# Performance work log

Hardware: AMD Instinct MI355X
Metric: run time of the kernel (lower is better)

## Reference

```python
import jax, jax.numpy as jnp
import numpy as np

N = 100000      # nodes
D = 128         # num_hidden_channels == num_output_feats
H = 4           # attention heads
HD = D // H     # head dim = 32
KNN = 20        # in-edges per node
E = N * KNN
BN_EPS = 1e-5


def setup_inputs() -> dict:
    key = jax.random.key(0)
    ks = jax.random.split(key, 20)
    s = 1.0 / np.sqrt(D)
    f = jax.random.normal(ks[0], (N, D), jnp.float32)
    src = jax.random.randint(ks[1], (E,), 0, N, dtype=jnp.int32)
    dst = jnp.repeat(jnp.arange(N, dtype=jnp.int32), KNN)  # knn in-edges per node
    return {
        "f": f,
        "src": src,
        "dst": dst,
        "bn1_gamma": jax.random.normal(ks[2], (D,), jnp.float32) * 0.1 + 1.0,
        "bn1_beta": jax.random.normal(ks[3], (D,), jnp.float32) * 0.1,
        "bn1_mean": jax.random.normal(ks[4], (D,), jnp.float32) * 0.1,
        "bn1_var": jax.random.uniform(ks[5], (D,), jnp.float32, 0.5, 1.5),
        "Wq": jax.random.normal(ks[6], (D, D), jnp.float32) * s,
        "Wk": jax.random.normal(ks[7], (D, D), jnp.float32) * s,
        "Wv": jax.random.normal(ks[8], (D, D), jnp.float32) * s,
        "Wo": jax.random.normal(ks[9], (D, D), jnp.float32) * s,
        "bo": jax.random.normal(ks[10], (D,), jnp.float32) * 0.01,
        "bn2_gamma": jax.random.normal(ks[11], (D,), jnp.float32) * 0.1 + 1.0,
        "bn2_beta": jax.random.normal(ks[12], (D,), jnp.float32) * 0.1,
        "bn2_mean": jax.random.normal(ks[13], (D,), jnp.float32) * 0.1,
        "bn2_var": jax.random.uniform(ks[14], (D,), jnp.float32, 0.5, 1.5),
        "W1": jax.random.normal(ks[15], (D, 2 * D), jnp.float32) * s,
        "W2": jax.random.normal(ks[16], (2 * D, D), jnp.float32) * (1.0 / np.sqrt(2 * D)),
    }


def _bn(x, gamma, beta, mean, var):
    # eval-mode BatchNorm1d with running statistics
    return (x - mean) * (gamma / jnp.sqrt(var + BN_EPS)) + beta


def reference(f, src, dst, bn1_gamma, bn1_beta, bn1_mean, bn1_var,
              Wq, Wk, Wv, Wo, bo,
              bn2_gamma, bn2_beta, bn2_mean, bn2_var, W1, W2):
    n = f.shape[0]
    h = _bn(f, bn1_gamma, bn1_beta, bn1_mean, bn1_var)
    q = (h @ Wq).reshape(n, H, HD)
    k = (h @ Wk).reshape(n, H, HD)
    v = (h @ Wv).reshape(n, H, HD)
    # edge-wise score: K[src] . Q[dst]  -> [E, H]
    score = jnp.einsum('ehd,ehd->eh', k[src], q[dst]) / np.sqrt(HD)
    score = jnp.exp(jnp.clip(score, -5.0, 5.0))
    # scatter-sum weighted V and normalizer to destination nodes
    wV = jax.ops.segment_sum(v[src] * score[:, :, None], dst, num_segments=n)  # [N,H,HD]
    z = jax.ops.segment_sum(score, dst, num_segments=n)                        # [N,H]
    attn = (wV / (z[:, :, None] + 1e-6)).reshape(n, D)
    node = attn @ Wo + bo
    node = f + node  # residual 1 (dropout is identity in eval)
    h2 = _bn(node, bn2_gamma, bn2_beta, bn2_mean, bn2_var)
    mlp = jax.nn.silu(h2 @ W1) @ W2
    return node + mlp  # residual 2
```

## Files before the change

kernel.cpp:

```cpp
#include <hip/hip_runtime.h>
#include <hip/hip_bf16.h>

#define NN 100000
#define DD 128
#define KNN 20

typedef unsigned short u16;
typedef __attribute__((ext_vector_type(8))) __bf16 bf16x8;
typedef __attribute__((ext_vector_type(4))) float f32x4;
typedef __attribute__((ext_vector_type(4))) unsigned short u16x4;
typedef __attribute__((ext_vector_type(8))) unsigned short u16x8;

__device__ __forceinline__ float b2f(u16 b) {
  unsigned int u = ((unsigned int)b) << 16;
  float f;
  __builtin_memcpy(&f, &u, 4);
  return f;
}
__device__ __forceinline__ u16 f2b(float f) {
  unsigned int u;
  __builtin_memcpy(&u, &f, 4);
  u += 0x7fffu + ((u >> 16) & 1u);
  return (u16)(u >> 16);
}

__global__ __launch_bounds__(256) void bn1_kernel(
    const float* __restrict__ f, const float* __restrict__ g, const float* __restrict__ be,
    const float* __restrict__ mu, const float* __restrict__ va, u16* __restrict__ h)
{
  int idx = (blockIdx.x * 256 + threadIdx.x) * 8;
  if (idx >= NN * DD) return;
  int c = idx & (DD - 1);
  u16x8 out;
#pragma unroll
  for (int j = 0; j < 8; j++) {
    float scale = g[c + j] * rsqrtf(va[c + j] + 1e-5f);
    out[j] = f2b((f[idx + j] - mu[c + j]) * scale + be[c + j]);
  }
  *(u16x8*)(h + idx) = out;
}

__device__ __forceinline__ void stage_frag(const float* __restrict__ W, int wstride,
                                           int colbase, u16* __restrict__ dst, int f) {
  int lane = f & 63;
  int t2 = f >> 6;
  int ksl = t2 & 3;
  int ct = (t2 >> 2) & 7;
  int kc = t2 >> 5;
  int ks = kc * 4 + ksl;
  int quad = lane >> 4, l16 = lane & 15;
  const float* src = W + (size_t)(ks * 32 + quad * 8) * wstride + colbase + ct * 16 + l16;
  u16x8 o;
#pragma unroll
  for (int j = 0; j < 8; j++) o[j] = f2b(src[(size_t)j * wstride]);
  *(u16x8*)(dst + (size_t)f * 8) = o;
}

__global__ __launch_bounds__(256) void stage_weights_kernel(
    const float* __restrict__ Wq, const float* __restrict__ Wk, const float* __restrict__ Wv,
    const float* __restrict__ Wo, const float* __restrict__ W1, const float* __restrict__ W2,
    u16* __restrict__ WTf)
{
  int t = blockIdx.x * 256 + threadIdx.x;
  if (t < 2048)       stage_frag(Wq, 128, 0,   WTf + 0,     t);
  else if (t < 4096)  stage_frag(Wk, 128, 0,   WTf + 16384, t - 2048);
  else if (t < 6144)  stage_frag(Wv, 128, 0,   WTf + 32768, t - 4096);
  else if (t < 8192)  stage_frag(Wo, 128, 0,   WTf + 49152, t - 6144);
  else if (t < 10240) stage_frag(W1, 256, 0,   WTf + 65536, t - 8192);
  else if (t < 12288) stage_frag(W1, 256, 128, WTf + 81920, t - 10240);
  else if (t < 16384) stage_frag(W2, 128, 0,   WTf + 98304, t - 12288);
}

template <int K, int NB, int MODE>
__global__ __launch_bounds__(256) void gemm3_kernel(
    const u16* __restrict__ A, const u16* __restrict__ Bf,
    u16* __restrict__ o0, u16* __restrict__ o1,
    float* __restrict__ of, float* __restrict__ nodef,
    const float* __restrict__ fres, const float* __restrict__ bo,
    const float* __restrict__ g2, const float* __restrict__ b2,
    const float* __restrict__ m2, const float* __restrict__ v2,
    const float* __restrict__ nodein, int nrows)
{
  constexpr int KS = K / 32;
  constexpr int NC = K / 128;
  __shared__ u16 Bs[16384];
  const int tid = threadIdx.x;
  const int wave = tid >> 6;
  const int lane = tid & 63;
  const int quad = lane >> 4;
  const int l16 = lane & 15;
  const int rowbase = blockIdx.x * 128 + wave * 32;

  bf16x8 a[2][KS];
#pragma unroll
  for (int rt = 0; rt < 2; rt++) {
    int arow = rowbase + rt * 16 + l16;
    if (arow >= nrows) arow = nrows - 1;
    const u16* Ap = A + (size_t)arow * K + quad * 8;
#pragma unroll
    for (int ks = 0; ks < KS; ks++) a[rt][ks] = *(const bf16x8*)(Ap + ks * 32);
  }

#pragma unroll
  for (int m = 0; m < NB; m++) {
    const u16* Bm = Bf + (size_t)m * (128 * K);
    f32x4 acc[2][8];
#pragma unroll
    for (int rt = 0; rt < 2; rt++)
#pragma unroll
      for (int ct = 0; ct < 8; ct++) acc[rt][ct] = (f32x4){0.f, 0.f, 0.f, 0.f};

#pragma unroll
    for (int kc = 0; kc < NC; kc++) {
      __syncthreads();
      const u16* srcp = Bm + kc * 16384 + tid * 8;
#pragma unroll
      for (int i = 0; i < 8; i++)
        *(u16x8*)(Bs + i * 2048 + tid * 8) = *(const u16x8*)(srcp + i * 2048);
      __syncthreads();
#pragma unroll
      for (int ct = 0; ct < 8; ct++) {
#pragma unroll
        for (int ksl = 0; ksl < 4; ksl++) {
          bf16x8 b = *(const bf16x8*)(Bs + ((ct * 4 + ksl) * 64 + lane) * 8);
          acc[0][ct] = __builtin_amdgcn_mfma_f32_16x16x32_bf16(a[0][kc * 4 + ksl], b, acc[0][ct], 0, 0, 0);
          acc[1][ct] = __builtin_amdgcn_mfma_f32_16x16x32_bf16(a[1][kc * 4 + ksl], b, acc[1][ct], 0, 0, 0);
        }
      }
    }

#pragma unroll
    for (int rt = 0; rt < 2; rt++) {
#pragma unroll
      for (int ct = 0; ct < 8; ct++) {
        int coll = ct * 16 + l16;
#pragma unroll
        for (int r = 0; r < 4; r++) {
          int row = rowbase + rt * 16 + quad * 4 + r;
          if (row >= nrows) continue;
          float val = acc[rt][ct][r];
          if (MODE == 0) {
            if (m == 0) o0[(size_t)row * DD + coll] = f2b(val);
            else if (m == 1) o1[(size_t)row * 256 + coll * 2] = f2b(val);
            else o1[(size_t)row * 256 + coll * 2 + 1] = f2b(val);
          } else if (MODE == 1) {
            float nv = val + bo[coll] + fres[(size_t)row * DD + coll];
            nodef[(size_t)row * DD + coll] = nv;
            float sc2 = g2[coll] * rsqrtf(v2[coll] + 1e-5f);
            o0[(size_t)row * DD + coll] = f2b((nv - m2[coll]) * sc2 + b2[coll]);
          } else if (MODE == 2) {
            int col = m * 128 + coll;
            float s = val / (1.f + __expf(-val));
            o0[(size_t)row * 256 + col] = f2b(s);
          } else {
            of[(size_t)row * DD + coll] = val + nodein[(size_t)row * DD + coll];
          }
        }
      }
    }
  }
}

__global__ __launch_bounds__(256) void attn_kernel(
    const u16* __restrict__ q, const u16* __restrict__ kv,
    const int* __restrict__ src, u16* __restrict__ attn)
{
  const int node = blockIdx.x * 8 + (threadIdx.x >> 5);
  const int sub = threadIdx.x & 31;
  const int c0 = sub * 4;
  const size_t qbase = (size_t)node * DD + c0;

  u16x4 qr = *(const u16x4*)(q + qbase);
  const float qv0 = b2f(qr[0]), qv1 = b2f(qr[1]), qv2 = b2f(qr[2]), qv3 = b2f(qr[3]);

  int sv[KNN];
  const int* sp = src + (size_t)node * KNN;
#pragma unroll
  for (int j = 0; j < KNN; j++) sv[j] = sp[j];

  float a0 = 0.f, a1 = 0.f, a2 = 0.f, a3 = 0.f, z = 0.f;
  const float inv_sqrt_hd = 0.17677669529663687f;
#pragma unroll
  for (int j = 0; j < KNN; j++) {
    u16x8 kvr = *(const u16x8*)(kv + (size_t)sv[j] * 256 + c0 * 2);
    float p = b2f(kvr[0]) * qv0 + b2f(kvr[2]) * qv1 + b2f(kvr[4]) * qv2 + b2f(kvr[6]) * qv3;
    p += __shfl_xor(p, 1);
    p += __shfl_xor(p, 2);
    p += __shfl_xor(p, 4);
    float sc = __expf(fminf(fmaxf(p * inv_sqrt_hd, -5.f), 5.f));
    z += sc;
    a0 += sc * b2f(kvr[1]);
    a1 += sc * b2f(kvr[3]);
    a2 += sc * b2f(kvr[5]);
    a3 += sc * b2f(kvr[7]);
  }
  float inv = 1.f / (z + 1e-6f);
  u16x4 o;
  o[0] = f2b(a0 * inv); o[1] = f2b(a1 * inv);
  o[2] = f2b(a2 * inv); o[3] = f2b(a3 * inv);
  *(u16x4*)(attn + qbase) = o;
}

extern "C" void kernel_launch(void* const* d_in, const int* in_sizes, int n_in,
                              void* d_out, int out_size, void* d_ws, size_t ws_size,
                              hipStream_t stream) {
  const float* f  = (const float*)d_in[0];
  const int* src  = (const int*)d_in[1];
  const float* g1 = (const float*)d_in[3];
  const float* b1 = (const float*)d_in[4];
  const float* m1 = (const float*)d_in[5];
  const float* v1 = (const float*)d_in[6];
  const float* Wq = (const float*)d_in[7];
  const float* Wk = (const float*)d_in[8];
  const float* Wv = (const float*)d_in[9];
  const float* Wo = (const float*)d_in[10];
  const float* bo = (const float*)d_in[11];
  const float* g2 = (const float*)d_in[12];
  const float* b2 = (const float*)d_in[13];
  const float* m2 = (const float*)d_in[14];
  const float* v2 = (const float*)d_in[15];
  const float* W1 = (const float*)d_in[16];
  const float* W2 = (const float*)d_in[17];
  float* out = (float*)d_out;

  char* ws = (char*)d_ws;
  const size_t SZ = (size_t)NN * DD * 2;
  u16*  h     = (u16*)(ws + 0);
  u16*  qb    = (u16*)(ws + SZ);
  u16*  kv    = (u16*)(ws + 2 * SZ);
  float* node = (float*)(ws + 4 * SZ);
  u16*  inter = (u16*)(ws + 2 * SZ);
  u16*  attn  = h;
  u16*  h2    = qb;
  u16*  WTf   = (u16*)(ws + 6 * SZ);

  const int g3grid = (NN + 127) / 128;

  bn1_kernel<<<(NN * DD / 8 + 255) / 256, 256, 0, stream>>>(f, g1, b1, m1, v1, h);
  stage_weights_kernel<<<64, 256, 0, stream>>>(Wq, Wk, Wv, Wo, W1, W2, WTf);

  gemm3_kernel<128, 3, 0><<<g3grid, 256, 0, stream>>>(
      h, WTf + 0, qb, kv, nullptr, nullptr,
      nullptr, nullptr, nullptr, nullptr, nullptr, nullptr, nullptr, NN);

  attn_kernel<<<NN / 8, 256, 0, stream>>>(qb, kv, src, attn);

  gemm3_kernel<128, 1, 1><<<g3grid, 256, 0, stream>>>(
      attn, WTf + 49152, h2, nullptr, nullptr, node,
      f, bo, g2, b2, m2, v2, nullptr, NN);

  gemm3_kernel<128, 2, 2><<<g3grid, 256, 0, stream>>>(
      h2, WTf + 65536, inter, nullptr, nullptr, nullptr,
      nullptr, nullptr, nullptr, nullptr, nullptr, nullptr, nullptr, NN);

  gemm3_kernel<256, 1, 3><<<g3grid, 256, 0, stream>>>(
      inter, WTf + 98304, nullptr, nullptr, out, nullptr,
      nullptr, nullptr, nullptr, nullptr, nullptr, nullptr, node, NN);
}
```

Measured before the change: 533.8 us.

## Fuse BN1 into QKV GEMM and fuse output, BN2 and MLP into one kernel

Folds BatchNorm1 into the QKV projection so the normalized activations are never written to memory, and fuses the Wo projection, residual, BN2, the SiLU MLP and the final residual into one kernel. The intermediate node and inter tensors stay in registers or per-wave shared-memory tiles instead of round-tripping through HBM. Weight fragments are now read straight from global/L2 instead of being staged into shared memory, and BN scale/bias are precomputed once. This removes several full-size intermediate reads and writes and some launches, in exchange for more register pressure in the fused MLP kernel and a partially unrolled attention loop.

Result: no change. 525.5 us (-1.6%).

```diff
diff --git a/kernel.cpp b/kernel.cpp
--- a/kernel.cpp
+++ b/kernel.cpp
@@ -22,22 +22,6 @@
   __builtin_memcpy(&u, &f, 4);
   u += 0x7fffu + ((u >> 16) & 1u);
   return (u16)(u >> 16);
-}
-
-__global__ __launch_bounds__(256) void bn1_kernel(
-    const float* __restrict__ f, const float* __restrict__ g, const float* __restrict__ be,
-    const float* __restrict__ mu, const float* __restrict__ va, u16* __restrict__ h)
-{
-  int idx = (blockIdx.x * 256 + threadIdx.x) * 8;
-  if (idx >= NN * DD) return;
-  int c = idx & (DD - 1);
-  u16x8 out;
-#pragma unroll
-  for (int j = 0; j < 8; j++) {
-    float scale = g[c + j] * rsqrtf(va[c + j] + 1e-5f);
-    out[j] = f2b((f[idx + j] - mu[c + j]) * scale + be[c + j]);
-  }
-  *(u16x8*)(h + idx) = out;
 }
 
 __device__ __forceinline__ void stage_frag(const float* __restrict__ W, int wstride,
@@ -59,7 +43,14 @@
 __global__ __launch_bounds__(256) void stage_weights_kernel(
     const float* __restrict__ Wq, const float* __restrict__ Wk, const float* __restrict__ Wv,
     const float* __restrict__ Wo, const float* __restrict__ W1, const float* __restrict__ W2,
-    u16* __restrict__ WTf)
+    const float* __restrict__ g1, const float* __restrict__ b1,
+    const float* __restrict__ m1, const float* __restrict__ v1,
+    const float* __restrict__ g2, const float* __restrict__ b2,
+    const float* __restrict__ m2, const float* __restrict__ v2,
+    const float* __restrict__ bo,
+    u16* __restrict__ WTf,
+    float* __restrict__ sc1, float* __restrict__ bb1,
+    float* __restrict__ sc2, float* __restrict__ bb2, float* __restrict__ bof)
 {
   int t = blockIdx.x * 256 + threadIdx.x;
   if (t < 2048)       stage_frag(Wq, 128, 0,   WTf + 0,     t);
@@ -69,101 +60,99 @@
   else if (t < 10240) stage_frag(W1, 256, 0,   WTf + 65536, t - 8192);
   else if (t < 12288) stage_frag(W1, 256, 128, WTf + 81920, t - 10240);
   else if (t < 16384) stage_frag(W2, 128, 0,   WTf + 98304, t - 12288);
-}
-
-template <int K, int NB, int MODE>
-__global__ __launch_bounds__(256) void gemm3_kernel(
-    const u16* __restrict__ A, const u16* __restrict__ Bf,
-    u16* __restrict__ o0, u16* __restrict__ o1,
-    float* __restrict__ of, float* __restrict__ nodef,
-    const float* __restrict__ fres, const float* __restrict__ bo,
-    const float* __restrict__ g2, const float* __restrict__ b2,
-    const float* __restrict__ m2, const float* __restrict__ v2,
-    const float* __restrict__ nodein, int nrows)
+  else if (t < 16512) {
+    int c = t - 16384;
+    float s1 = g1[c] * rsqrtf(v1[c] + 1e-5f);
+    sc1[c] = s1; bb1[c] = b1[c] - m1[c] * s1;
+    float s2 = g2[c] * rsqrtf(v2[c] + 1e-5f);
+    sc2[c] = s2; bb2[c] = b2[c] - m2[c] * s2;
+    bof[c] = bo[c];
+  }
+}
+
+__global__ __launch_bounds__(256) void qkv_kernel(
+    const float* __restrict__ f, const u16* __restrict__ WTf,
+    const float* __restrict__ sc1, const float* __restrict__ bb1,
+    u16* __restrict__ qb, u16* __restrict__ kvb)
 {
-  constexpr int KS = K / 32;
-  constexpr int NC = K / 128;
-  __shared__ u16 Bs[16384];
   const int tid = threadIdx.x;
-  const int wave = tid >> 6;
-  const int lane = tid & 63;
-  const int quad = lane >> 4;
-  const int l16 = lane & 15;
+  const int wave = tid >> 6, lane = tid & 63, quad = lane >> 4, l16 = lane & 15;
   const int rowbase = blockIdx.x * 128 + wave * 32;
 
-  bf16x8 a[2][KS];
-#pragma unroll
-  for (int rt = 0; rt < 2; rt++) {
-    int arow = rowbase + rt * 16 + l16;
-    if (arow >= nrows) arow = nrows - 1;
-    const u16* Ap = A + (size_t)arow * K + quad * 8;
-#pragma unroll
-    for (int ks = 0; ks < KS; ks++) a[rt][ks] = *(const bf16x8*)(Ap + ks * 32);
-  }
-
-#pragma unroll
-  for (int m = 0; m < NB; m++) {
-    const u16* Bm = Bf + (size_t)m * (128 * K);
+  bf16x8 af[2][4];
+#pragma unroll
+  for (int ks = 0; ks < 4; ks++) {
+    int ch = ks * 32 + quad * 8;
+    f32x4 s0 = *(const f32x4*)(sc1 + ch), s1 = *(const f32x4*)(sc1 + ch + 4);
+    f32x4 c0 = *(const f32x4*)(bb1 + ch), c1 = *(const f32x4*)(bb1 + ch + 4);
+#pragma unroll
+    for (int rt = 0; rt < 2; rt++) {
+      int arow = rowbase + rt * 16 + l16;
+      if (arow >= NN) arow = NN - 1;
+      const float* fp = f + (size_t)arow * DD + ch;
+      f32x4 x0 = *(const f32x4*)(fp), x1 = *(const f32x4*)(fp + 4);
+      u16x8 hv;
+#pragma unroll
+      for (int j = 0; j < 4; j++) {
+        hv[j]     = f2b(x0[j] * s0[j] + c0[j]);
+        hv[j + 4] = f2b(x1[j] * s1[j] + c1[j]);
+      }
+      af[rt][ks] = __builtin_bit_cast(bf16x8, hv);
+    }
+  }
+
+  u16x4 ks16[2][8];
+#pragma unroll
+  for (int m = 0; m < 3; m++) {
     f32x4 acc[2][8];
 #pragma unroll
     for (int rt = 0; rt < 2; rt++)
 #pragma unroll
       for (int ct = 0; ct < 8; ct++) acc[rt][ct] = (f32x4){0.f, 0.f, 0.f, 0.f};
-
-#pragma unroll
-    for (int kc = 0; kc < NC; kc++) {
-      __syncthreads();
-      const u16* srcp = Bm + kc * 16384 + tid * 8;
-#pragma unroll
-      for (int i = 0; i < 8; i++)
-        *(u16x8*)(Bs + i * 2048 + tid * 8) = *(const u16x8*)(srcp + i * 2048);
-      __syncthreads();
+#pragma unroll
+    for (int ct = 0; ct < 8; ct++)
+#pragma unroll
+      for (int ks = 0; ks < 4; ks++) {
+        bf16x8 wf = *(const bf16x8*)(WTf + (size_t)m * 16384 + ((ct * 4 + ks) * 64 + lane) * 8);
+        acc[0][ct] = __builtin_amdgcn_mfma_f32_16x16x32_bf16(wf, af[0][ks], acc[0][ct], 0, 0, 0);
+        acc[1][ct] = __builtin_amdgcn_mfma_f32_16x16x32_bf16(wf, af[1][ks], acc[1][ct], 0, 0, 0);
+      }
+#pragma unroll
+    for (int rt = 0; rt < 2; rt++)
 #pragma unroll
       for (int ct = 0; ct < 8; ct++) {
-#pragma unroll
-        for (int ksl = 0; ksl < 4; ksl++) {
-          bf16x8 b = *(const bf16x8*)(Bs + ((ct * 4 + ksl) * 64 + lane) * 8);
-          acc[0][ct] = __builtin_amdgcn_mfma_f32_16x16x32_bf16(a[0][kc * 4 + ksl], b, acc[0][ct], 0, 0, 0);
-          acc[1][ct] = __builtin_amdgcn_mfma_f32_16x16x32_bf16(a[1][kc * 4 + ksl], b, acc[1][ct], 0, 0, 0);
-        }
-      }
-    }
-
-#pragma unroll
-    for (int rt = 0; rt < 2; rt++) {
-#pragma unroll
-      for (int ct = 0; ct < 8; ct++) {
-        int coll = ct * 16 + l16;
-#pragma unroll
-        for (int r = 0; r < 4; r++) {
-          int row = rowbase + rt * 16 + quad * 4 + r;
-          if (row >= nrows) continue;
-          float val = acc[rt][ct][r];
-          if (MODE == 0) {
-            if (m == 0) o0[(size_t)row * DD + coll] = f2b(val);
-            else if (m == 1) o1[(size_t)row * 256 + coll * 2] = f2b(val);
-            else o1[(size_t)row * 256 + coll * 2 + 1] = f2b(val);
-          } else if (MODE == 1) {
-            float nv = val + bo[coll] + fres[(size_t)row * DD + coll];
-            nodef[(size_t)row * DD + coll] = nv;
-            float sc2 = g2[coll] * rsqrtf(v2[coll] + 1e-5f);
-            o0[(size_t)row * DD + coll] = f2b((nv - m2[coll]) * sc2 + b2[coll]);
-          } else if (MODE == 2) {
-            int col = m * 128 + coll;
-            float s = val / (1.f + __expf(-val));
-            o0[(size_t)row * 256 + col] = f2b(s);
-          } else {
-            of[(size_t)row * DD + coll] = val + nodein[(size_t)row * DD + coll];
+        int row = rowbase + rt * 16 + l16;
+        int ch0 = ct * 16 + quad * 4;
+        if (m == 0) {
+          if (row < NN) {
+            u16x4 o;
+#pragma unroll
+            for (int r = 0; r < 4; r++) o[r] = f2b(acc[rt][ct][r]);
+            *(u16x4*)(qb + (size_t)row * DD + ch0) = o;
+          }
+        } else if (m == 1) {
+          u16x4 o;
+#pragma unroll
+          for (int r = 0; r < 4; r++) o[r] = f2b(acc[rt][ct][r]);
+          ks16[rt][ct] = o;
+        } else {
+          if (row < NN) {
+            u16x8 o;
+#pragma unroll
+            for (int r = 0; r < 4; r++) {
+              o[2 * r] = ks16[rt][ct][r];
+              o[2 * r + 1] = f2b(acc[rt][ct][r]);
+            }
+            *(u16x8*)(kvb + (size_t)row * 256 + ch0 * 2) = o;
           }
         }
       }
-    }
   }
 }
 
 __global__ __launch_bounds__(256) void attn_kernel(
     const u16* __restrict__ q, const u16* __restrict__ kv,
-    const int* __restrict__ src, u16* __restrict__ attn)
+    const int* __restrict__ src, u16* __restrict__ attnb)
 {
   const int node = blockIdx.x * 8 + (threadIdx.x >> 5);
   const int sub = threadIdx.x & 31;
@@ -180,7 +169,7 @@
 
   float a0 = 0.f, a1 = 0.f, a2 = 0.f, a3 = 0.f, z = 0.f;
   const float inv_sqrt_hd = 0.17677669529663687f;
-#pragma unroll
+#pragma unroll 10
   for (int j = 0; j < KNN; j++) {
     u16x8 kvr = *(const u16x8*)(kv + (size_t)sv[j] * 256 + c0 * 2);
     float p = b2f(kvr[0]) * qv0 + b2f(kvr[2]) * qv1 + b2f(kvr[4]) * qv2 + b2f(kvr[6]) * qv3;
@@ -198,7 +187,134 @@
   u16x4 o;
   o[0] = f2b(a0 * inv); o[1] = f2b(a1 * inv);
   o[2] = f2b(a2 * inv); o[3] = f2b(a3 * inv);
-  *(u16x4*)(attn + qbase) = o;
+  *(u16x4*)(attnb + qbase) = o;
+}
+
+__global__ __launch_bounds__(256) void mlp_kernel(
+    const u16* __restrict__ attnb, const float* __restrict__ f, const u16* __restrict__ WTf,
+    const float* __restrict__ bof, const float* __restrict__ sc2, const float* __restrict__ bb2,
+    float* __restrict__ out)
+{
+  __shared__ u16 T[8704];
+  const int tid = threadIdx.x;
+  const int wave = tid >> 6, lane = tid & 63, quad = lane >> 4, l16 = lane & 15;
+  const int rowbase = blockIdx.x * 128 + wave * 32;
+  u16* tile = T + wave * 2176;
+
+  bf16x8 af[2][4];
+#pragma unroll
+  for (int rt = 0; rt < 2; rt++) {
+    int arow = rowbase + rt * 16 + l16;
+    if (arow >= NN) arow = NN - 1;
+    const u16* ap = attnb + (size_t)arow * DD + quad * 8;
+#pragma unroll
+    for (int ks = 0; ks < 4; ks++) af[rt][ks] = *(const bf16x8*)(ap + ks * 32);
+  }
+
+  f32x4 nv[2][8];
+#pragma unroll
+  for (int rt = 0; rt < 2; rt++)
+#pragma unroll
+    for (int ct = 0; ct < 8; ct++) nv[rt][ct] = (f32x4){0.f, 0.f, 0.f, 0.f};
+#pragma unroll
+  for (int ct = 0; ct < 8; ct++)
+#pragma unroll
+    for (int ks = 0; ks < 4; ks++) {
+      bf16x8 wf = *(const bf16x8*)(WTf + 49152 + ((ct * 4 + ks) * 64 + lane) * 8);
+      nv[0][ct] = __builtin_amdgcn_mfma_f32_16x16x32_bf16(wf, af[0][ks], nv[0][ct], 0, 0, 0);
+      nv[1][ct] = __builtin_amdgcn_mfma_f32_16x16x32_bf16(wf, af[1][ks], nv[1][ct], 0, 0, 0);
+    }
+
+  u16x4 h4s[8];
+#pragma unroll
+  for (int ct = 0; ct < 8; ct++) {
+    int ch0 = ct * 16 + quad * 4;
+    f32x4 bo4 = *(const f32x4*)(bof + ch0);
+    f32x4 s4  = *(const f32x4*)(sc2 + ch0);
+    f32x4 b4  = *(const f32x4*)(bb2 + ch0);
+#pragma unroll
+    for (int rt = 0; rt < 2; rt++) {
+      int row = rowbase + rt * 16 + l16;
+      int rl = row < NN ? row : NN - 1;
+      f32x4 f4 = *(const f32x4*)(f + (size_t)rl * DD + ch0);
+      nv[rt][ct] += bo4 + f4;
+      u16x4 h4;
+#pragma unroll
+      for (int r = 0; r < 4; r++) h4[r] = f2b(nv[rt][ct][r] * s4[r] + b4[r]);
+      if (rt == 0) *(u16x4*)(tile + l16 * 136 + ch0) = h4;
+      else h4s[ct] = h4;
+    }
+  }
+  bf16x8 hf[2][4];
+#pragma unroll
+  for (int ks = 0; ks < 4; ks++) hf[0][ks] = *(const bf16x8*)(tile + l16 * 136 + ks * 32 + quad * 8);
+#pragma unroll
+  for (int ct = 0; ct < 8; ct++) *(u16x4*)(tile + l16 * 136 + ct * 16 + quad * 4) = h4s[ct];
+#pragma unroll
+  for (int ks = 0; ks < 4; ks++) hf[1][ks] = *(const bf16x8*)(tile + l16 * 136 + ks * 32 + quad * 8);
+
+  f32x4 acc3[2][8];
+#pragma unroll
+  for (int rt = 0; rt < 2; rt++)
+#pragma unroll
+    for (int ct = 0; ct < 8; ct++) acc3[rt][ct] = (f32x4){0.f, 0.f, 0.f, 0.f};
+
+#pragma unroll
+  for (int m = 0; m < 2; m++) {
+    f32x4 acc2[2][8];
+#pragma unroll
+    for (int rt = 0; rt < 2; rt++)
+#pragma unroll
+      for (int ct = 0; ct < 8; ct++) acc2[rt][ct] = (f32x4){0.f, 0.f, 0.f, 0.f};
+#pragma unroll
+    for (int ct = 0; ct < 8; ct++)
+#pragma unroll
+      for (int ks = 0; ks < 4; ks++) {
+        bf16x8 wf = *(const bf16x8*)(WTf + 65536 + m * 16384 + ((ct * 4 + ks) * 64 + lane) * 8);
+        acc2[0][ct] = __builtin_amdgcn_mfma_f32_16x16x32_bf16(wf, hf[0][ks], acc2[0][ct], 0, 0, 0);
+        acc2[1][ct] = __builtin_amdgcn_mfma_f32_16x16x32_bf16(wf, hf[1][ks], acc2[1][ct], 0, 0, 0);
+      }
+    u16x4 i4s[8];
+#pragma unroll
+    for (int ct = 0; ct < 8; ct++) {
+      int ch0 = ct * 16 + quad * 4;
+      u16x4 i0, i1;
+#pragma unroll
+      for (int r = 0; r < 4; r++) {
+        float x0 = acc2[0][ct][r], x1 = acc2[1][ct][r];
+        i0[r] = f2b(x0 / (1.f + __expf(-x0)));
+        i1[r] = f2b(x1 / (1.f + __expf(-x1)));
+      }
+      *(u16x4*)(tile + l16 * 136 + ch0) = i0;
+      i4s[ct] = i1;
+    }
+    bf16x8 iff[2][4];
+#pragma unroll
+    for (int ksl = 0; ksl < 4; ksl++) iff[0][ksl] = *(const bf16x8*)(tile + l16 * 136 + ksl * 32 + quad * 8);
+#pragma unroll
+    for (int ct = 0; ct < 8; ct++) *(u16x4*)(tile + l16 * 136 + ct * 16 + quad * 4) = i4s[ct];
+#pragma unroll
+    for (int ksl = 0; ksl < 4; ksl++) iff[1][ksl] = *(const bf16x8*)(tile + l16 * 136 + ksl * 32 + quad * 8);
+#pragma unroll
+    for (int ct = 0; ct < 8; ct++)
+#pragma unroll
+      for (int ksl = 0; ksl < 4; ksl++) {
+        bf16x8 wf = *(const bf16x8*)(WTf + 98304 + ((m * 32 + ct * 4 + ksl) * 64 + lane) * 8);
+        acc3[0][ct] = __builtin_amdgcn_mfma_f32_16x16x32_bf16(wf, iff[0][ksl], acc3[0][ct], 0, 0, 0);
+        acc3[1][ct] = __builtin_amdgcn_mfma_f32_16x16x32_bf16(wf, iff[1][ksl], acc3[1][ct], 0, 0, 0);
+      }
+  }
+
+#pragma unroll
+  for (int rt = 0; rt < 2; rt++)
+#pragma unroll
+    for (int ct = 0; ct < 8; ct++) {
+      int row = rowbase + rt * 16 + l16;
+      if (row < NN) {
+        int ch0 = ct * 16 + quad * 4;
+        *(f32x4*)(out + (size_t)row * DD + ch0) = acc3[rt][ct] + nv[rt][ct];
+      }
+    }
 }
 
 extern "C" void kernel_launch(void* const* d_in, const int* in_sizes, int n_in,
@@ -224,36 +340,25 @@
   float* out = (float*)d_out;
 
   char* ws = (char*)d_ws;
-  const size_t SZ = (size_t)NN * DD * 2;
-  u16*  h     = (u16*)(ws + 0);
-  u16*  qb    = (u16*)(ws + SZ);
-  u16*  kv    = (u16*)(ws + 2 * SZ);
-  float* node = (float*)(ws + 4 * SZ);
-  u16*  inter = (u16*)(ws + 2 * SZ);
-  u16*  attn  = h;
-  u16*  h2    = qb;
-  u16*  WTf   = (u16*)(ws + 6 * SZ);
-
-  const int g3grid = (NN + 127) / 128;
-
-  bn1_kernel<<<(NN * DD / 8 + 255) / 256, 256, 0, stream>>>(f, g1, b1, m1, v1, h);
-  stage_weights_kernel<<<64, 256, 0, stream>>>(Wq, Wk, Wv, Wo, W1, W2, WTf);
-
-  gemm3_kernel<128, 3, 0><<<g3grid, 256, 0, stream>>>(
-      h, WTf + 0, qb, kv, nullptr, nullptr,
-      nullptr, nullptr, nullptr, nullptr, nullptr, nullptr, nullptr, NN);
-
-  attn_kernel<<<NN / 8, 256, 0, stream>>>(qb, kv, src, attn);
-
-  gemm3_kernel<128, 1, 1><<<g3grid, 256, 0, stream>>>(
-      attn, WTf + 49152, h2, nullptr, nullptr, node,
-      f, bo, g2, b2, m2, v2, nullptr, NN);
-
-  gemm3_kernel<128, 2, 2><<<g3grid, 256, 0, stream>>>(
-      h2, WTf + 65536, inter, nullptr, nullptr, nullptr,
-      nullptr, nullptr, nullptr, nullptr, nullptr, nullptr, nullptr, NN);
-
-  gemm3_kernel<256, 1, 3><<<g3grid, 256, 0, stream>>>(
-      inter, WTf + 98304, nullptr, nullptr, out, nullptr,
-      nullptr, nullptr, nullptr, nullptr, nullptr, nullptr, node, NN);
-}
+  u16*  WTf = (u16*)(ws + 0);
+  float* sc1 = (float*)(ws + 262144);
+  float* bb1 = (float*)(ws + 262656);
+  float* sc2 = (float*)(ws + 263168);
+  float* bb2 = (float*)(ws + 263680);
+  float* bof = (float*)(ws + 264192);
+  u16*  qb    = (u16*)(ws + 1048576);
+  u16*  kvb   = (u16*)(ws + 26648576);
+  u16*  attnb = (u16*)(ws + 77848576);
+
+  const int ggrid = (NN + 127) / 128;
+
+  stage_weights_kernel<<<65, 256, 0, stream>>>(
+      Wq, Wk, Wv, Wo, W1, W2, g1, b1, m1, v1, g2, b2, m2, v2, bo,
+      WTf, sc1, bb1, sc2, bb2, bof);
+
+  qkv_kernel<<<ggrid, 256, 0, stream>>>(f, WTf, sc1, bb1, qb, kvb);
+
+  attn_kernel<<<NN / 8, 256, 0, stream>>>(qb, kvb, src, attnb);
+
+  mlp_kernel<<<ggrid, 256, 0, stream>>>(attnb, f, WTf, bof, sc2, bb2, out);
+}
```
